# Optimization experiments

Hardware: AMD Instinct MI355X
Metric: run time of the kernel (lower is better)

## Reference

```python
import jax, jax.numpy as jnp
import numpy as np

B, T, C, H = 16, 2048, 192, 64

def setup_inputs() -> dict:
    key = jax.random.key(0)
    k1, k2, k3, k4 = jax.random.split(key, 4)
    x = jax.random.normal(k1, (B, T, C), dtype=jnp.float32)
    Wq = jax.random.normal(k2, (C, H), dtype=jnp.float32) * (C ** -0.5)
    Wk = jax.random.normal(k3, (C, H), dtype=jnp.float32) * (C ** -0.5)
    Wv = jax.random.normal(k4, (C, H), dtype=jnp.float32) * (C ** -0.5)
    return {"x": x, "Wq": Wq, "Wk": Wk, "Wv": Wv}

def reference(x, Wq, Wk, Wv):
    # One head of causal self-attention (dropout in eval mode / identity).
    q = x @ Wq                       # [B, T, H]
    k = x @ Wk                       # [B, T, H]
    v = x @ Wv                       # [B, T, H]
    scale = q.shape[-1] ** -0.5
    wei = jnp.einsum('bth,bsh->bts', q, k) * scale   # [B, T, T]
    t = wei.shape[-1]
    causal = jnp.tril(jnp.ones((t, t), dtype=bool))  # tril mask
    wei = jnp.where(causal, wei, -jnp.inf)
    wei = jax.nn.softmax(wei, axis=-1)
    out = jnp.einsum('bts,bsh->bth', wei, v)         # [B, T, H]
    return out
```

## Files before the change

kernel.cpp:

```cpp
#include <hip/hip_runtime.h>

#define B 16
#define T 2048
#define C 192
#define H 64

typedef __bf16 bf16x8 __attribute__((ext_vector_type(8)));
typedef __bf16 bf16x4 __attribute__((ext_vector_type(4)));
typedef float  f32x4  __attribute__((ext_vector_type(4)));

#define MFMA(a, b, c) __builtin_amdgcn_mfma_f32_16x16x32_bf16(a, b, c, 0, 0, 0)

#define SM_BIAS 24.0f

__global__ __launch_bounds__(256) void wtrans_kernel(
    const float* __restrict__ Wq, const float* __restrict__ Wk,
    const float* __restrict__ Wv, __bf16* __restrict__ wt)
{
    const int idx = blockIdx.x * 256 + threadIdx.x;
    const int n = idx / C;
    const int k = idx - n * C;
    const float* W = (n < 64) ? Wq : (n < 128) ? Wk : Wv;
    const int nc = n & 63;
    wt[n * C + k] = (__bf16)W[k * H + nc];
}

__global__ __launch_bounds__(256) void qkv_mfma_kernel(
    const float* __restrict__ x, const __bf16* __restrict__ wt,
    __bf16* __restrict__ qb, __bf16* __restrict__ kb, __bf16* __restrict__ vt)
{
    __shared__ __bf16 tile[64][72];

    const int tid  = threadIdx.x;
    const int w    = tid >> 6;
    const int l    = tid & 63;
    const int lid  = l & 15;
    const int quad = l >> 4;
    const int m0   = blockIdx.x * 64 + w * 16;

    f32x4 acc[12] = {};
    const float* xrow = x + (size_t)(m0 + lid) * C + quad * 8;

    #pragma unroll
    for (int kc = 0; kc < 6; kc++) {
        const float4 a0 = *(const float4*)(xrow + kc * 32);
        const float4 a1 = *(const float4*)(xrow + kc * 32 + 4);
        bf16x8 af;
        af[0] = (__bf16)a0.x; af[1] = (__bf16)a0.y;
        af[2] = (__bf16)a0.z; af[3] = (__bf16)a0.w;
        af[4] = (__bf16)a1.x; af[5] = (__bf16)a1.y;
        af[6] = (__bf16)a1.z; af[7] = (__bf16)a1.w;
        const __bf16* wb = wt + kc * 32 + quad * 8 + lid * C;
        #pragma unroll
        for (int nt = 0; nt < 12; nt++) {
            const bf16x8 bf = *(const bf16x8*)(wb + nt * 16 * C);
            acc[nt] = MFMA(af, bf, acc[nt]);
        }
    }

    #pragma unroll
    for (int nt = 0; nt < 8; nt++) {
        const int n = nt * 16 + lid;
        __bf16* dst = (n < 64) ? qb : kb;
        const int col = n & 63;
        const float scale = (n < 64) ? 0.1803368801111204f : 1.0f;
        #pragma unroll
        for (int r = 0; r < 4; r++) {
            const int row = m0 + quad * 4 + r;
            dst[(size_t)row * H + col] = (__bf16)(acc[nt][r] * scale);
        }
    }

    #pragma unroll
    for (int nt = 8; nt < 12; nt++) {
        const int col = (nt - 8) * 16 + lid;
        #pragma unroll
        for (int r = 0; r < 4; r++)
            tile[w * 16 + quad * 4 + r][col] = (__bf16)(acc[nt][r]);
    }
    __syncthreads();

    const int bb = blockIdx.x >> 5;
    const int t0 = (blockIdx.x & 31) << 6;
    #pragma unroll
    for (int it = 0; it < 2; ++it) {
        const int h   = it * 32 + (tid >> 3);
        const int tl0 = (tid & 7) * 8;
        bf16x8 d;
        #pragma unroll
        for (int j = 0; j < 8; j++) d[j] = tile[tl0 + j][h];
        *(bf16x8*)(vt + ((size_t)(bb * H + h)) * T + t0 + tl0) = d;
    }
}

__global__ __launch_bounds__(256) void attn_kernel(
    const __bf16* __restrict__ qb,
    const __bf16* __restrict__ kb,
    const __bf16* __restrict__ vt,
    float* __restrict__ out)
{
    __shared__ __bf16 Kb[2][64][72];
    __shared__ __bf16 Vb[2][64][72];

    const int tid  = threadIdx.x;
    const int w    = tid >> 6;
    const int l    = tid & 63;
    const int lid  = l & 15;
    const int quad = l >> 4;

    const int b   = blockIdx.x & 15;
    const int qt  = 31 - (blockIdx.x >> 4);
    const int q0  = qt << 6;
    const int qw0 = q0 + w * 16;
    const int nch = qt + 1;
    const size_t bbase = (size_t)b * T;

    const __bf16* qrow = qb + (bbase + qw0 + lid) * H + quad * 8;
    const bf16x8 qf0 = *(const bf16x8*)(qrow);
    const bf16x8 qf1 = *(const bf16x8*)(qrow + 32);

    f32x4 O[4] = {};
    float lsum = 0.f;

    const __bf16* kgb = kb + bbase * H;
    const __bf16* vgb = vt + (size_t)b * H * T;

    const int pa = tid, pb = tid + 256;
    const int ra = pa >> 3, ca = (pa & 7) * 8;
    const int rb = pb >> 3, cb = (pb & 7) * 8;

    bf16x8 kra, krb, vra, vrb;
    auto prefetch = [&](int key0) {
        kra = *(const bf16x8*)(kgb + (size_t)(key0 + ra) * H + ca);
        krb = *(const bf16x8*)(kgb + (size_t)(key0 + rb) * H + cb);
        vra = *(const bf16x8*)(vgb + (size_t)ra * T + key0 + ca);
        vrb = *(const bf16x8*)(vgb + (size_t)rb * T + key0 + cb);
    };

    prefetch(0);
    int cur = 0;
    for (int kt = 0; kt < nch; kt++) {
        *(bf16x8*)&Kb[cur][ra][ca] = kra;
        *(bf16x8*)&Kb[cur][rb][cb] = krb;
        *(bf16x8*)&Vb[cur][ra][ca] = vra;
        *(bf16x8*)&Vb[cur][rb][cb] = vrb;
        __syncthreads();
        if (kt + 1 < nch) prefetch((kt + 1) << 6);

        const int key0 = kt << 6;

        bf16x8 kf[8];
        #pragma unroll
        for (int j = 0; j < 4; j++) {
            kf[2 * j]     = *(const bf16x8*)&Kb[cur][j * 16 + lid][quad * 8];
            kf[2 * j + 1] = *(const bf16x8*)&Kb[cur][j * 16 + lid][32 + quad * 8];
        }

        bf16x8 af0, af1;
        const bool boundary = (key0 + 63 > qw0);
        #pragma unroll
        for (int j = 0; j < 4; j++) {
            f32x4 s = {-SM_BIAS, -SM_BIAS, -SM_BIAS, -SM_BIAS};
            s = MFMA(kf[2 * j], qf0, s);
            s = MFMA(kf[2 * j + 1], qf1, s);
            if (boundary) {
                #pragma unroll
                for (int r = 0; r < 4; r++)
                    if (key0 + j * 16 + quad * 4 + r > qw0 + lid) s[r] = -1e30f;
            }
            #pragma unroll
            for (int r = 0; r < 4; r++) {
                const float p = __builtin_amdgcn_exp2f(s[r]);
                lsum += p;
                if      (j == 0) af0[r]     = (__bf16)p;
                else if (j == 1) af0[4 + r] = (__bf16)p;
                else if (j == 2) af1[r]     = (__bf16)p;
                else             af1[4 + r] = (__bf16)p;
            }
        }

        #pragma unroll
        for (int ht = 0; ht < 4; ht++) {
            const __bf16* vr = &Vb[cur][ht * 16 + lid][quad * 4];
            bf16x8 bv0, bv1;
            ((bf16x4*)&bv0)[0] = *(const bf16x4*)(vr);
            ((bf16x4*)&bv0)[1] = *(const bf16x4*)(vr + 16);
            ((bf16x4*)&bv1)[0] = *(const bf16x4*)(vr + 32);
            ((bf16x4*)&bv1)[1] = *(const bf16x4*)(vr + 48);
            O[ht] = MFMA(af0, bv0, O[ht]);
            O[ht] = MFMA(af1, bv1, O[ht]);
        }
        cur ^= 1;
    }

    lsum += __shfl_xor(lsum, 16, 64);
    lsum += __shfl_xor(lsum, 32, 64);

    #pragma unroll
    for (int ht = 0; ht < 4; ht++)
        #pragma unroll
        for (int r = 0; r < 4; r++) {
            const float Lr = __shfl(lsum, quad * 4 + r, 16);
            out[(bbase + qw0 + quad * 4 + r) * H + ht * 16 + lid] = O[ht][r] / Lr;
        }
}

extern "C" void kernel_launch(void* const* d_in, const int* in_sizes, int n_in,
                              void* d_out, int out_size, void* d_ws, size_t ws_size,
                              hipStream_t stream)
{
    const float* x  = (const float*)d_in[0];
    const float* Wq = (const float*)d_in[1];
    const float* Wk = (const float*)d_in[2];
    const float* Wv = (const float*)d_in[3];

    const size_t BTH = (size_t)B * T * H;
    __bf16* qbuf = (__bf16*)d_ws;
    __bf16* kbuf = qbuf + BTH;
    __bf16* vtb  = kbuf + BTH;
    __bf16* wt   = vtb + BTH;
    float* outp = (float*)d_out;

    wtrans_kernel<<<(C * 3 * H) / 256, 256, 0, stream>>>(Wq, Wk, Wv, wt);
    qkv_mfma_kernel<<<B * T / 64, 256, 0, stream>>>(x, wt, qbuf, kbuf, vtb);
    attn_kernel<<<B * T / 64, 256, 0, stream>>>(qbuf, kbuf, vtb, outp);
}
```

Before: 125.4 us.

## Pair causal query tiles per block and stage QKV weights in LDS

Measured after the change: 114.0 us. 9.1% less time.

```diff
diff --git a/kernel.cpp b/kernel.cpp
--- a/kernel.cpp
+++ b/kernel.cpp
@@ -29,33 +29,57 @@
     const float* __restrict__ x, const __bf16* __restrict__ wt,
     __bf16* __restrict__ qb, __bf16* __restrict__ kb, __bf16* __restrict__ vt)
 {
+    __shared__ __bf16 Ws[2][192][40];
     __shared__ __bf16 tile[64][72];
 
     const int tid  = threadIdx.x;
     const int w    = tid >> 6;
-    const int l    = tid & 63;
-    const int lid  = l & 15;
-    const int quad = l >> 4;
+    const int lid  = tid & 15;
+    const int quad = (tid & 63) >> 4;
     const int m0   = blockIdx.x * 64 + w * 16;
 
+    const float* xrow = x + (size_t)(m0 + lid) * C + quad * 8;
+    float4 a0[6], a1[6];
+    #pragma unroll
+    for (int kc = 0; kc < 6; kc++) {
+        a0[kc] = *(const float4*)(xrow + kc * 32);
+        a1[kc] = *(const float4*)(xrow + kc * 32 + 4);
+    }
+    bf16x8 af[6];
+    #pragma unroll
+    for (int kc = 0; kc < 6; kc++) {
+        af[kc][0] = (__bf16)a0[kc].x; af[kc][1] = (__bf16)a0[kc].y;
+        af[kc][2] = (__bf16)a0[kc].z; af[kc][3] = (__bf16)a0[kc].w;
+        af[kc][4] = (__bf16)a1[kc].x; af[kc][5] = (__bf16)a1[kc].y;
+        af[kc][6] = (__bf16)a1[kc].z; af[kc][7] = (__bf16)a1[kc].w;
+    }
+
+    bf16x8 wpf[3];
+    auto prefW = [&](int kc) {
+        #pragma unroll
+        for (int i = 0; i < 3; i++) {
+            const int p = i * 256 + tid;
+            wpf[i] = *(const bf16x8*)(wt + (p >> 2) * C + kc * 32 + (p & 3) * 8);
+        }
+    };
+
     f32x4 acc[12] = {};
-    const float* xrow = x + (size_t)(m0 + lid) * C + quad * 8;
-
-    #pragma unroll
+    prefW(0);
+    int cur = 0;
     for (int kc = 0; kc < 6; kc++) {
-        const float4 a0 = *(const float4*)(xrow + kc * 32);
-        const float4 a1 = *(const float4*)(xrow + kc * 32 + 4);
-        bf16x8 af;
-        af[0] = (__bf16)a0.x; af[1] = (__bf16)a0.y;
-        af[2] = (__bf16)a0.z; af[3] = (__bf16)a0.w;
-        af[4] = (__bf16)a1.x; af[5] = (__bf16)a1.y;
-        af[6] = (__bf16)a1.z; af[7] = (__bf16)a1.w;
-        const __bf16* wb = wt + kc * 32 + quad * 8 + lid * C;
+        #pragma unroll
+        for (int i = 0; i < 3; i++) {
+            const int p = i * 256 + tid;
+            *(bf16x8*)&Ws[cur][p >> 2][(p & 3) * 8] = wpf[i];
+        }
+        __syncthreads();
+        if (kc < 5) prefW(kc + 1);
         #pragma unroll
         for (int nt = 0; nt < 12; nt++) {
-            const bf16x8 bf = *(const bf16x8*)(wb + nt * 16 * C);
-            acc[nt] = MFMA(af, bf, acc[nt]);
-        }
+            const bf16x8 bfr = *(const bf16x8*)&Ws[cur][nt * 16 + lid][quad * 8];
+            acc[nt] = MFMA(af[kc], bfr, acc[nt]);
+        }
+        cur ^= 1;
     }
 
     #pragma unroll
@@ -104,30 +128,31 @@
 
     const int tid  = threadIdx.x;
     const int w    = tid >> 6;
-    const int l    = tid & 63;
-    const int lid  = l & 15;
-    const int quad = l >> 4;
+    const int lid  = tid & 15;
+    const int quad = (tid & 63) >> 4;
 
     const int b   = blockIdx.x & 15;
-    const int qt  = 31 - (blockIdx.x >> 4);
-    const int q0  = qt << 6;
-    const int qw0 = q0 + w * 16;
-    const int nch = qt + 1;
+    const int pr  = blockIdx.x >> 4;
+    const int qtH = 31 - pr, qtL = pr;
+    const int nchH = qtH + 1;
+    const int ntot = 33;
     const size_t bbase = (size_t)b * T;
 
-    const __bf16* qrow = qb + (bbase + qw0 + lid) * H + quad * 8;
-    const bf16x8 qf0 = *(const bf16x8*)(qrow);
-    const bf16x8 qf1 = *(const bf16x8*)(qrow + 32);
-
-    f32x4 O[4] = {};
-    float lsum = 0.f;
+    const int qH = (qtH << 6) + w * 16;
+    const int qL = (qtL << 6) + w * 16;
+
+    const __bf16* qrH = qb + (bbase + qH + lid) * H + quad * 8;
+    const bf16x8 qfH0 = *(const bf16x8*)(qrH);
+    const bf16x8 qfH1 = *(const bf16x8*)(qrH + 32);
+    const __bf16* qrL = qb + (bbase + qL + lid) * H + quad * 8;
+    const bf16x8 qfL0 = *(const bf16x8*)(qrL);
+    const bf16x8 qfL1 = *(const bf16x8*)(qrL + 32);
 
     const __bf16* kgb = kb + bbase * H;
     const __bf16* vgb = vt + (size_t)b * H * T;
 
-    const int pa = tid, pb = tid + 256;
-    const int ra = pa >> 3, ca = (pa & 7) * 8;
-    const int rb = pb >> 3, cb = (pb & 7) * 8;
+    const int ra = tid >> 3,         ca = (tid & 7) * 8;
+    const int rb = (tid + 256) >> 3, cb = (tid & 7) * 8;
 
     bf16x8 kra, krb, vra, vrb;
     auto prefetch = [&](int key0) {
@@ -136,18 +161,47 @@
         vra = *(const bf16x8*)(vgb + (size_t)ra * T + key0 + ca);
         vrb = *(const bf16x8*)(vgb + (size_t)rb * T + key0 + cb);
     };
+    auto keyof = [&](int i) { return (i < nchH ? i : i - nchH) << 6; };
+
+    f32x4 O[4] = {};
+    float lsum = 0.f;
+
+    auto epilogue = [&](int qw0) {
+        float ls = lsum;
+        ls += __shfl_xor(ls, 16, 64);
+        ls += __shfl_xor(ls, 32, 64);
+        #pragma unroll
+        for (int ht = 0; ht < 4; ht++)
+            #pragma unroll
+            for (int r = 0; r < 4; r++) {
+                const float Lr = __shfl(ls, quad * 4 + r, 16);
+                out[(bbase + qw0 + quad * 4 + r) * H + ht * 16 + lid] =
+                    O[ht][r] / Lr;
+            }
+    };
+
+    bf16x8 cq0 = qfH0, cq1 = qfH1;
+    int cqw = qH;
 
     prefetch(0);
     int cur = 0;
-    for (int kt = 0; kt < nch; kt++) {
+    for (int i = 0; i < ntot; i++) {
         *(bf16x8*)&Kb[cur][ra][ca] = kra;
         *(bf16x8*)&Kb[cur][rb][cb] = krb;
         *(bf16x8*)&Vb[cur][ra][ca] = vra;
         *(bf16x8*)&Vb[cur][rb][cb] = vrb;
         __syncthreads();
-        if (kt + 1 < nch) prefetch((kt + 1) << 6);
-
-        const int key0 = kt << 6;
+        if (i + 1 < ntot) prefetch(keyof(i + 1));
+
+        if (i == nchH) {
+            epilogue(cqw);
+            #pragma unroll
+            for (int ht = 0; ht < 4; ht++) O[ht] = (f32x4){0.f, 0.f, 0.f, 0.f};
+            lsum = 0.f;
+            cq0 = qfL0; cq1 = qfL1; cqw = qL;
+        }
+
+        const int key0 = keyof(i);
 
         bf16x8 kf[8];
         #pragma unroll
@@ -157,16 +211,16 @@
         }
 
         bf16x8 af0, af1;
-        const bool boundary = (key0 + 63 > qw0);
+        const bool boundary = (key0 + 63 > cqw);
         #pragma unroll
         for (int j = 0; j < 4; j++) {
             f32x4 s = {-SM_BIAS, -SM_BIAS, -SM_BIAS, -SM_BIAS};
-            s = MFMA(kf[2 * j], qf0, s);
-            s = MFMA(kf[2 * j + 1], qf1, s);
+            s = MFMA(kf[2 * j], cq0, s);
+            s = MFMA(kf[2 * j + 1], cq1, s);
             if (boundary) {
                 #pragma unroll
                 for (int r = 0; r < 4; r++)
-                    if (key0 + j * 16 + quad * 4 + r > qw0 + lid) s[r] = -1e30f;
+                    if (key0 + j * 16 + quad * 4 + r > cqw + lid) s[r] = -1e30f;
             }
             #pragma unroll
             for (int r = 0; r < 4; r++) {
@@ -192,17 +246,7 @@
         }
         cur ^= 1;
     }
-
-    lsum += __shfl_xor(lsum, 16, 64);
-    lsum += __shfl_xor(lsum, 32, 64);
-
-    #pragma unroll
-    for (int ht = 0; ht < 4; ht++)
-        #pragma unroll
-        for (int r = 0; r < 4; r++) {
-            const float Lr = __shfl(lsum, quad * 4 + r, 16);
-            out[(bbase + qw0 + quad * 4 + r) * H + ht * 16 + lid] = O[ht][r] / Lr;
-        }
+    epilogue(cqw);
 }
 
 extern "C" void kernel_launch(void* const* d_in, const int* in_sizes, int n_in,
@@ -223,5 +267,5 @@
 
     wtrans_kernel<<<(C * 3 * H) / 256, 256, 0, stream>>>(Wq, Wk, Wv, wt);
     qkv_mfma_kernel<<<B * T / 64, 256, 0, stream>>>(x, wt, qbuf, kbuf, vtb);
-    attn_kernel<<<B * T / 64, 256, 0, stream>>>(qbuf, kbuf, vtb, outp);
-}
+    attn_kernel<<<B * T / 128, 256, 0, stream>>>(qbuf, kbuf, vtb, outp);
+}
```
